# Optimization experiments

Hardware: AMD Instinct MI355X
Metric: run time of the kernel (lower is better)

The kernel has to match this reference:

```python
import jax, jax.numpy as jnp
import numpy as np

EPS_RMS = 1e-6
EPS_L2 = 1e-12  # torch F.normalize default eps


def _l2_normalize(x):
    n = jnp.sqrt(jnp.sum(x * x, axis=-1, keepdims=True))
    return x / jnp.maximum(n, EPS_L2)


def _dwconv(x, w, b):
    # depthwise Conv1d: x [B,L,D], w [D,1,K], b [D]; padding=K//2 (same length for odd K)
    K = w.shape[-1]
    y = jax.lax.conv_general_dilated(
        jnp.swapaxes(x, 1, 2), w, window_strides=(1,),
        padding=[(K // 2, K // 2)], feature_group_count=w.shape[0],
        dimension_numbers=('NCH', 'OIH', 'NCH'))
    return jnp.swapaxes(y + b[None, :, None], 1, 2)


def setup_inputs() -> dict:
    key = jax.random.key(0)
    ks = jax.random.split(key, 12)
    B, L, D, K = 8, 2048, 128, 3
    inp = {
        'x': jax.random.normal(ks[0], (B, L, D), dtype=jnp.float32),
        'state': jnp.zeros((B, D, D), dtype=jnp.float32),
        'W_in': jax.random.normal(ks[1], (4 * D, D), dtype=jnp.float32) * 0.02,
        'W_gate': jax.random.normal(ks[2], (2 * D, D), dtype=jnp.float32) * 0.02,
        'W_out': jax.random.normal(ks[3], (D, D), dtype=jnp.float32) * 0.02,
        'W_res': jax.random.normal(ks[4], (D, D), dtype=jnp.float32) * 0.02,
        'qconv_w': jax.random.normal(ks[5], (D, 1, K), dtype=jnp.float32) * 0.5,
        'qconv_b': jnp.zeros((D,), dtype=jnp.float32),
        'kconv_w': jax.random.normal(ks[6], (D, 1, K), dtype=jnp.float32) * 0.5,
        'kconv_b': jnp.zeros((D,), dtype=jnp.float32),
        'rms_w': jnp.ones((D,), dtype=jnp.float32),
    }
    return inp


def reference(x, state, W_in, W_gate, W_out, W_res,
              qconv_w, qconv_b, kconv_w, kconv_b, rms_w):
    B, L, D = x.shape
    residual = x @ W_res.T
    qkv = x @ W_in.T  # [B,L,4D]
    q, k, v, gate = jnp.split(qkv, 4, axis=-1)
    q = _l2_normalize(jax.nn.sigmoid(_dwconv(q, qconv_w, qconv_b)))
    k = _l2_normalize(jax.nn.sigmoid(_dwconv(k, kconv_w, kconv_b)))
    g = jax.nn.sigmoid(gate @ W_gate.T)  # [B,L,2D]
    alpha, beta = jnp.split(g, 2, axis=-1)

    # Delta-rule recurrence over time. State S [B,D,D] indexed S[b, v_dim, k_dim]:
    # S <- alpha_j * (S_ij - (S k)_i * beta_j k_j) + beta_j * v_i k_j ; out = silu(q @ S)
    def step(S, inp):
        q_t, k_t, v_t, a_t, b_t = inp  # each [B,D]
        Sk = jnp.einsum('bij,bj->bi', S, k_t)          # S @ k
        bk = b_t * k_t                                  # beta*k, column scaling
        S = a_t[:, None, :] * (S - Sk[:, :, None] * bk[:, None, :]) \
            + v_t[:, :, None] * bk[:, None, :]
        out_t = jax.nn.silu(jnp.einsum('bi,bij->bj', q_t, S))
        return S, out_t

    xs = tuple(jnp.swapaxes(a, 0, 1) for a in (q, k, v, alpha, beta))  # [L,B,D]
    S_fin, outs = jax.lax.scan(step, state, xs)
    out = jnp.swapaxes(outs, 0, 1) @ W_out.T  # [B,L,D]
    # dropout (p=0.125) is identity in eval mode
    out = out * jax.lax.rsqrt(jnp.mean(out * out, axis=-1, keepdims=True) + EPS_RMS) * rms_w
    out = out + residual
    return out, S_fin
```

## Files before the change

### kernel.cpp

```cpp
#include <hip/hip_runtime.h>
#include <hip/hip_bf16.h>
#include <math.h>

#define BB 8
#define LL 2048
#define LQ 512
#define DD 128

template <int CTRL>
__device__ __forceinline__ float dpp_add(float x) {
    int xi = __float_as_int(x);
    int yi = __builtin_amdgcn_update_dpp(xi, xi, CTRL, 0xF, 0xF, false);
    return x + __int_as_float(yi);
}
__device__ __forceinline__ float allreduce16(float p) {
    p = dpp_add<0xB1>(p);
    p = dpp_add<0x4E>(p);
    p = dpp_add<0x141>(p);
    p = dpp_add<0x140>(p);
    return p;
}
__device__ __forceinline__ float rlane(float p, int l) {
    return __int_as_float(__builtin_amdgcn_readlane(__float_as_int(p), l));
}

__global__ __launch_bounds__(256) void gemm_kernel(
    const float* __restrict__ X, long ldx, long sB, long sQ,
    const float* __restrict__ W,
    float* __restrict__ C, int ldc,
    int applySig)
{
    __shared__ float Xs[32 * 132];
    __shared__ float Ws[64 * 132];
    const int tid = threadIdx.x;
    const int m0 = blockIdx.x * 32;
    const int o0 = blockIdx.y * 64;
    {
        int row = tid >> 3, cg = tid & 7;
        int m = m0 + row;
        int b = m >> 11, t = m & 2047, qq = t >> 9, tl = t & 511;
        const float* src = X + (size_t)b * sB + (size_t)qq * sQ
                             + (size_t)tl * ldx + cg * 16;
        float* dst = Xs + row * 132 + cg * 16;
#pragma unroll
        for (int u = 0; u < 4; ++u)
            *(float4*)(dst + 4 * u) = *(const float4*)(src + 4 * u);
    }
    {
        int o = tid >> 2, cg = tid & 3;
        const float* src = W + (size_t)(o0 + o) * 128 + cg * 32;
        float* dst = Ws + o * 132 + cg * 32;
#pragma unroll
        for (int u = 0; u < 8; ++u)
            *(float4*)(dst + 4 * u) = *(const float4*)(src + 4 * u);
    }
    __syncthreads();
    const int tx = tid & 31, ty = tid >> 5;
    float acc[4][2] = {};
    const float* xb = Xs + (ty * 4) * 132;
    const float* wb = Ws + (tx * 2) * 132;
    for (int k0 = 0; k0 < 128; k0 += 4) {
        float4 xr[4], wr[2];
#pragma unroll
        for (int r = 0; r < 4; ++r) xr[r] = *(const float4*)(xb + r * 132 + k0);
#pragma unroll
        for (int cc = 0; cc < 2; ++cc) wr[cc] = *(const float4*)(wb + cc * 132 + k0);
#pragma unroll
        for (int r = 0; r < 4; ++r)
#pragma unroll
            for (int cc = 0; cc < 2; ++cc) {
                acc[r][cc] += xr[r].x * wr[cc].x + xr[r].y * wr[cc].y
                            + xr[r].z * wr[cc].z + xr[r].w * wr[cc].w;
            }
    }
#pragma unroll
    for (int r = 0; r < 4; ++r)
#pragma unroll
        for (int cc = 0; cc < 2; ++cc) {
            float v = acc[r][cc];
            if (applySig) v = 1.0f / (1.0f + __expf(-v));
            C[(size_t)(m0 + ty * 4 + r) * ldc + o0 + tx * 2 + cc] = v;
        }
}

__global__ __launch_bounds__(256) void convnorm_kernel(
    const float* __restrict__ qkv,
    const float* __restrict__ qw, const float* __restrict__ qb,
    const float* __restrict__ kw, const float* __restrict__ kb,
    const float* __restrict__ ab,
    float* __restrict__ pack)
{
    const int tid = threadIdx.x;
    const int lane = tid & 63;
    const int wid = tid >> 6;
    const int m = blockIdx.x * 4 + wid;
    const int l = m & (LL - 1);
    const int b = m >> 11;
    const int d0 = lane * 2;
    float yq0 = qb[d0], yq1 = qb[d0 + 1];
    float yk0 = kb[d0], yk1 = kb[d0 + 1];
#pragma unroll
    for (int tau = 0; tau < 3; ++tau) {
        int lp = l + tau - 1;
        if (lp >= 0 && lp < LL) {
            const float* base = qkv + (size_t)(m + tau - 1) * 512;
            yq0 += base[d0]       * qw[d0 * 3 + tau];
            yq1 += base[d0 + 1]   * qw[(d0 + 1) * 3 + tau];
            yk0 += base[128 + d0]     * kw[d0 * 3 + tau];
            yk1 += base[128 + d0 + 1] * kw[(d0 + 1) * 3 + tau];
        }
    }
    yq0 = 1.0f / (1.0f + __expf(-yq0));
    yq1 = 1.0f / (1.0f + __expf(-yq1));
    yk0 = 1.0f / (1.0f + __expf(-yk0));
    yk1 = 1.0f / (1.0f + __expf(-yk1));
    float sq = yq0 * yq0 + yq1 * yq1;
    float sk = yk0 * yk0 + yk1 * yk1;
#pragma unroll
    for (int msk = 1; msk <= 32; msk <<= 1) {
        sq += __shfl_xor(sq, msk);
        sk += __shfl_xor(sk, msk);
    }
    float rq = 1.0f / fmaxf(sqrtf(sq), 1e-12f);
    float rk = 1.0f / fmaxf(sqrtf(sk), 1e-12f);
    float k0n = yk0 * rk, k1n = yk1 * rk;
    float a0 = ab[(size_t)m * 256 + d0];
    float a1 = ab[(size_t)m * 256 + d0 + 1];
    float b0 = ab[(size_t)m * 256 + 128 + d0];
    float b1 = ab[(size_t)m * 256 + 128 + d0 + 1];
    float v0 = qkv[(size_t)m * 512 + 256 + d0];
    float v1 = qkv[(size_t)m * 512 + 256 + d0 + 1];
    float* P = pack + ((size_t)b * 512 + (l >> 2)) * 2560 + (l & 3);
    P[d0 * 4]              = k0n;      P[(d0 + 1) * 4]        = k1n;
    P[512 + d0 * 4]        = b0 * k0n; P[512 + (d0 + 1) * 4]  = b1 * k1n;
    P[1024 + d0 * 4]       = a0;       P[1024 + (d0 + 1) * 4] = a1;
    P[1536 + d0 * 4]       = yq0 * rq; P[1536 + (d0 + 1) * 4] = yq1 * rq;
    P[2048 + d0 * 4]       = v0;       P[2048 + (d0 + 1) * 4] = v1;
}

__global__ __launch_bounds__(64, 1) void recur1_kernel(
    const float* __restrict__ pack, const float* __restrict__ sin,
    __hip_bfloat16* __restrict__ pout, float* __restrict__ sout, int blk0)
{
    const int lane = threadIdx.x;
    const int b = blockIdx.x >> 7;
    const int g = blockIdx.x & 127;
    const int j0 = lane * 2;

    float SA[2];
    {
        const float* sp = sin + ((size_t)b * DD + g) * DD + j0;
        float2 t2 = *(const float2*)sp;
        SA[0] = t2.x; SA[1] = t2.y;
    }

    const float* P = pack + ((size_t)b * 512 + blk0) * 2560;
    __hip_bfloat16* po = pout + ((size_t)g * (BB * LQ) + (size_t)b * LQ) * DD + j0;

    float4 ka4[2][2], ma4[2][2], aa4[2][2];
    float4 qv4[2], vv4[2];

#define PREB(BF)                                                             \
    do {                                                                     \
        ka4[BF][0] = *(const float4*)(P + j0 * 4);                           \
        ka4[BF][1] = *(const float4*)(P + j0 * 4 + 4);                       \
        ma4[BF][0] = *(const float4*)(P + 512 + j0 * 4);                     \
        ma4[BF][1] = *(const float4*)(P + 512 + j0 * 4 + 4);                 \
        aa4[BF][0] = *(const float4*)(P + 1024 + j0 * 4);                    \
        aa4[BF][1] = *(const float4*)(P + 1024 + j0 * 4 + 4);                \
        qv4[BF]    = *(const float4*)(P + 1536 + g * 4);                     \
        vv4[BF]    = *(const float4*)(P + 2048 + g * 4);                     \
        P += 2560;                                                           \
        __builtin_amdgcn_sched_barrier(0);         \
    } while (0)

#define STEPQ(BF, CMP)                                                       \
    do {                                                                     \
        float e = SA[0] * ka4[BF][0].CMP;                                    \
        e = fmaf(SA[1], ka4[BF][1].CMP, e);                                  \
        float p = allreduce16(e);                                            \
        float sk = (rlane(p, 0) + rlane(p, 16))                              \
                 + (rlane(p, 32) + rlane(p, 48));                            \
        float vg = vv4[BF].CMP, qg = qv4[BF].CMP;                            \
        float a0 = aa4[BF][0].CMP, a1 = aa4[BF][1].CMP;                      \
        float w0 = fmaf(-a0, sk, vg);                                        \
        SA[0] = fmaf(ma4[BF][0].CMP, w0, a0 * SA[0]);                        \
        float w1 = fmaf(-a1, sk, vg);                                        \
        SA[1] = fmaf(ma4[BF][1].CMP, w1, a1 * SA[1]);                        \
        __hip_bfloat162 h2;                                                  \
        h2.x = __float2bfloat16(qg * SA[0]);                                 \
        h2.y = __float2bfloat16(qg * SA[1]);                                 \
        *(__hip_bfloat162*)po = h2;                                          \
        po += DD;                                                            \
    } while (0)

#define STEP4(BF) \
    do { STEPQ(BF, x); STEPQ(BF, y); STEPQ(BF, z); STEPQ(BF, w); } while (0)

    PREB(0);
    PREB(1);
    for (int tb = 0; tb < LQ / 4; tb += 2) {
        STEP4(0);
        PREB(0);
        STEP4(1);
        PREB(1);
    }
#undef PREB
#undef STEPQ
#undef STEP4

    {
        float* sp = sout + ((size_t)b * DD + g) * DD + j0;
        float2 o2 = {SA[0], SA[1]};
        *(float2*)sp = o2;
    }
}

__global__ __launch_bounds__(256) void combine_silu_kernel(
    const ushort* __restrict__ pout, float* __restrict__ ocbase, int q)
{
    const size_t NQ = (size_t)BB * LQ * DD;
    size_t idx = ((size_t)blockIdx.x * 256 + threadIdx.x) * 4;
    float s0 = 0, s1 = 0, s2 = 0, s3 = 0;
#pragma unroll 8
    for (int gi = 0; gi < 128; ++gi) {
        uint2 u = *(const uint2*)(pout + gi * NQ + idx);
        s0 += __uint_as_float((u.x & 0xffffu) << 16);
        s1 += __uint_as_float(u.x & 0xffff0000u);
        s2 += __uint_as_float((u.y & 0xffffu) << 16);
        s3 += __uint_as_float(u.y & 0xffff0000u);
    }
    float4 r;
    r.x = s0 / (1.0f + __expf(-s0));
    r.y = s1 / (1.0f + __expf(-s1));
    r.z = s2 / (1.0f + __expf(-s2));
    r.w = s3 / (1.0f + __expf(-s3));
    size_t b = idx >> 16;
    size_t rem = idx & ((size_t)LQ * DD - 1);
    float* dst = ocbase + b * (512ull * 2560) + (size_t)q * (128ull * 2560) + rem;
    *(float4*)dst = r;
}

__global__ __launch_bounds__(256) void rms_res_kernel(
    const float* __restrict__ y, const float* __restrict__ res,
    const float* __restrict__ rmsw, float* __restrict__ out)
{
    const int tid = threadIdx.x;
    const int lane = tid & 63;
    const int wid = tid >> 6;
    const int m = blockIdx.x * 4 + wid;
    const int d0 = lane * 2;
    size_t o = (size_t)m * DD + d0;
    float2 yv = *(const float2*)(y + o);
    float ss = yv.x * yv.x + yv.y * yv.y;
#pragma unroll
    for (int msk = 1; msk <= 32; msk <<= 1) ss += __shfl_xor(ss, msk);
    float r = rsqrtf(ss * (1.0f / 128.0f) + 1e-6f);
    float2 rv = *(const float2*)(res + o);
    out[o]     = yv.x * r * rmsw[d0]     + rv.x;
    out[o + 1] = yv.y * r * rmsw[d0 + 1] + rv.y;
}

extern "C" void kernel_launch(void* const* d_in, const int* in_sizes, int n_in,
                              void* d_out, int out_size, void* d_ws, size_t ws_size,
                              hipStream_t stream)
{
    const float* x      = (const float*)d_in[0];
    const float* state  = (const float*)d_in[1];
    const float* W_in   = (const float*)d_in[2];
    const float* W_gate = (const float*)d_in[3];
    const float* W_out  = (const float*)d_in[4];
    const float* W_res  = (const float*)d_in[5];
    const float* qcw    = (const float*)d_in[6];
    const float* qcb    = (const float*)d_in[7];
    const float* kcw    = (const float*)d_in[8];
    const float* kcb    = (const float*)d_in[9];
    const float* rmsw   = (const float*)d_in[10];
    float* out  = (float*)d_out;
    float* sfin = out + (size_t)BB * LL * DD;

    const size_t M = (size_t)BB * LL;
    char* base = (char*)d_ws;
    const size_t PACK_BYTES = M * 640 * 4;
    float* pack = (float*)base;
    char*  poreg = base + PACK_BYTES;
    float* qkv = (float*)poreg;
    float* abv = (float*)(poreg + M * 512 * 4);
    __hip_bfloat16* po = (__hip_bfloat16*)poreg;
    float* res = (float*)poreg;
    float* yb  = (float*)(poreg + M * DD * 4);

    dim3 blk(256);
    gemm_kernel<<<dim3(M / 32, 8), blk, 0, stream>>>(
        x, 128, 2048L * 128, 512L * 128, W_in, qkv, 512, 0);
    gemm_kernel<<<dim3(M / 32, 4), blk, 0, stream>>>(
        qkv + 384, 512, 2048L * 512, 512L * 512, W_gate, abv, 256, 1);
    convnorm_kernel<<<dim3(M / 4), blk, 0, stream>>>(qkv, qcw, qcb, kcw, kcb, abv, pack);
    for (int q = 0; q < 4; ++q) {
        const float* sin = (q == 0) ? state : sfin;
        recur1_kernel<<<dim3(BB * 128), dim3(64), 0, stream>>>(
            pack, sin, po, sfin, q * 128);
        combine_silu_kernel<<<dim3(512), blk, 0, stream>>>(
            (const ushort*)po, pack, q);
    }
    gemm_kernel<<<dim3(M / 32, 2), blk, 0, stream>>>(
        x, 128, 2048L * 128, 512L * 128, W_res, res, 128, 0);
    gemm_kernel<<<dim3(M / 32, 2), blk, 0, stream>>>(
        pack, 128, 512L * 2560, 128L * 2560, W_out, yb, 128, 0);
    rms_res_kernel<<<dim3(M / 4), blk, 0, stream>>>(yb, res, rmsw, out);
}
```

Baseline: 562.7 us.

## Process two state rows per wave and split recurrence into two halves

The recurrence kernel now has each 64-lane block own two rows of the state instead of one, so 512 blocks run in place of 1024. Each k/alpha/beta load and each step's bookkeeping is shared across both rows, and the two rows' partial outputs are summed before the bf16 store. The sequence is cut into 2 chunks of 1024 steps instead of 4 chunks of 512, which halves the recurrence and combine launches and halves the partial-output buffer the combine kernel reads. In exchange there is less block-level parallelism and a longer serial dependence chain per launch. Chunk and stride indexing in the GEMM and combine kernels are updated to match.

```diff
diff --git a/kernel.cpp b/kernel.cpp
--- a/kernel.cpp
+++ b/kernel.cpp
@@ -4,7 +4,7 @@
 
 #define BB 8
 #define LL 2048
-#define LQ 512
+#define LH 1024
 #define DD 128
 
 template <int CTRL>
@@ -25,7 +25,7 @@
 }
 
 __global__ __launch_bounds__(256) void gemm_kernel(
-    const float* __restrict__ X, long ldx, long sB, long sQ,
+    const float* __restrict__ X, long ldx, long sB, long sH,
     const float* __restrict__ W,
     float* __restrict__ C, int ldc,
     int applySig)
@@ -38,8 +38,8 @@
     {
         int row = tid >> 3, cg = tid & 7;
         int m = m0 + row;
-        int b = m >> 11, t = m & 2047, qq = t >> 9, tl = t & 511;
-        const float* src = X + (size_t)b * sB + (size_t)qq * sQ
+        int b = m >> 11, t = m & 2047, h = t >> 10, tl = t & 1023;
+        const float* src = X + (size_t)b * sB + (size_t)h * sH
                              + (size_t)tl * ldx + cg * 16;
         float* dst = Xs + row * 132 + cg * 16;
 #pragma unroll
@@ -138,27 +138,31 @@
     P[2048 + d0 * 4]       = v0;       P[2048 + (d0 + 1) * 4] = v1;
 }
 
-__global__ __launch_bounds__(64, 1) void recur1_kernel(
+__global__ __launch_bounds__(64, 1) void recur2c_kernel(
     const float* __restrict__ pack, const float* __restrict__ sin,
     __hip_bfloat16* __restrict__ pout, float* __restrict__ sout, int blk0)
 {
     const int lane = threadIdx.x;
-    const int b = blockIdx.x >> 7;
-    const int g = blockIdx.x & 127;
+    const int b = blockIdx.x >> 6;
+    const int g = blockIdx.x & 63;
+    const int r0 = g * 2;
     const int j0 = lane * 2;
 
-    float SA[2];
+    float S0[2], S1[2];
     {
-        const float* sp = sin + ((size_t)b * DD + g) * DD + j0;
+        const float* sp = sin + ((size_t)b * DD + r0) * DD + j0;
         float2 t2 = *(const float2*)sp;
-        SA[0] = t2.x; SA[1] = t2.y;
+        S0[0] = t2.x; S0[1] = t2.y;
+        sp += DD;
+        t2 = *(const float2*)sp;
+        S1[0] = t2.x; S1[1] = t2.y;
     }
 
     const float* P = pack + ((size_t)b * 512 + blk0) * 2560;
-    __hip_bfloat16* po = pout + ((size_t)g * (BB * LQ) + (size_t)b * LQ) * DD + j0;
+    __hip_bfloat16* po = pout + ((size_t)g * (BB * LH) + (size_t)b * LH) * DD + j0;
 
     float4 ka4[2][2], ma4[2][2], aa4[2][2];
-    float4 qv4[2], vv4[2];
+    float4 qv4[2][2], vv4[2][2];
 
 #define PREB(BF)                                                             \
     do {                                                                     \
@@ -168,28 +172,38 @@
         ma4[BF][1] = *(const float4*)(P + 512 + j0 * 4 + 4);                 \
         aa4[BF][0] = *(const float4*)(P + 1024 + j0 * 4);                    \
         aa4[BF][1] = *(const float4*)(P + 1024 + j0 * 4 + 4);                \
-        qv4[BF]    = *(const float4*)(P + 1536 + g * 4);                     \
-        vv4[BF]    = *(const float4*)(P + 2048 + g * 4);                     \
+        qv4[BF][0] = *(const float4*)(P + 1536 + r0 * 4);                    \
+        qv4[BF][1] = *(const float4*)(P + 1536 + r0 * 4 + 4);                \
+        vv4[BF][0] = *(const float4*)(P + 2048 + r0 * 4);                    \
+        vv4[BF][1] = *(const float4*)(P + 2048 + r0 * 4 + 4);                \
         P += 2560;                                                           \
         __builtin_amdgcn_sched_barrier(0);         \
     } while (0)
 
 #define STEPQ(BF, CMP)                                                       \
     do {                                                                     \
-        float e = SA[0] * ka4[BF][0].CMP;                                    \
-        e = fmaf(SA[1], ka4[BF][1].CMP, e);                                  \
-        float p = allreduce16(e);                                            \
-        float sk = (rlane(p, 0) + rlane(p, 16))                              \
-                 + (rlane(p, 32) + rlane(p, 48));                            \
-        float vg = vv4[BF].CMP, qg = qv4[BF].CMP;                            \
+        float k0 = ka4[BF][0].CMP, k1 = ka4[BF][1].CMP;                      \
+        float e0 = S0[0] * k0; e0 = fmaf(S0[1], k1, e0);                     \
+        float e1 = S1[0] * k0; e1 = fmaf(S1[1], k1, e1);                     \
+        float p0 = allreduce16(e0);                                          \
+        float p1 = allreduce16(e1);                                          \
+        float sk0 = (rlane(p0, 0) + rlane(p0, 16))                           \
+                  + (rlane(p0, 32) + rlane(p0, 48));                         \
+        float sk1 = (rlane(p1, 0) + rlane(p1, 16))                           \
+                  + (rlane(p1, 32) + rlane(p1, 48));                         \
+        float v0 = vv4[BF][0].CMP, v1 = vv4[BF][1].CMP;                      \
+        float q0 = qv4[BF][0].CMP, q1 = qv4[BF][1].CMP;                      \
         float a0 = aa4[BF][0].CMP, a1 = aa4[BF][1].CMP;                      \
-        float w0 = fmaf(-a0, sk, vg);                                        \
-        SA[0] = fmaf(ma4[BF][0].CMP, w0, a0 * SA[0]);                        \
-        float w1 = fmaf(-a1, sk, vg);                                        \
-        SA[1] = fmaf(ma4[BF][1].CMP, w1, a1 * SA[1]);                        \
+        float m0 = ma4[BF][0].CMP, m1 = ma4[BF][1].CMP;                      \
+        float t00 = fmaf(-a0, sk0, v0); S0[0] = fmaf(m0, t00, a0 * S0[0]);   \
+        float t10 = fmaf(-a0, sk1, v1); S1[0] = fmaf(m0, t10, a0 * S1[0]);   \
+        float t01 = fmaf(-a1, sk0, v0); S0[1] = fmaf(m1, t01, a1 * S0[1]);   \
+        float t11 = fmaf(-a1, sk1, v1); S1[1] = fmaf(m1, t11, a1 * S1[1]);   \
+        float po0 = fmaf(q1, S1[0], q0 * S0[0]);                             \
+        float po1 = fmaf(q1, S1[1], q0 * S0[1]);                             \
         __hip_bfloat162 h2;                                                  \
-        h2.x = __float2bfloat16(qg * SA[0]);                                 \
-        h2.y = __float2bfloat16(qg * SA[1]);                                 \
+        h2.x = __float2bfloat16(po0);                                        \
+        h2.y = __float2bfloat16(po1);                                        \
         *(__hip_bfloat162*)po = h2;                                          \
         po += DD;                                                            \
     } while (0)
@@ -199,7 +213,7 @@
 
     PREB(0);
     PREB(1);
-    for (int tb = 0; tb < LQ / 4; tb += 2) {
+    for (int tb = 0; tb < LH / 4; tb += 2) {
         STEP4(0);
         PREB(0);
         STEP4(1);
@@ -210,21 +224,24 @@
 #undef STEP4
 
     {
-        float* sp = sout + ((size_t)b * DD + g) * DD + j0;
-        float2 o2 = {SA[0], SA[1]};
+        float* sp = sout + ((size_t)b * DD + r0) * DD + j0;
+        float2 o2 = {S0[0], S0[1]};
         *(float2*)sp = o2;
+        sp += DD;
+        float2 o3 = {S1[0], S1[1]};
+        *(float2*)sp = o3;
     }
 }
 
 __global__ __launch_bounds__(256) void combine_silu_kernel(
-    const ushort* __restrict__ pout, float* __restrict__ ocbase, int q)
-{
-    const size_t NQ = (size_t)BB * LQ * DD;
+    const ushort* __restrict__ pout, float* __restrict__ ocbase, int h)
+{
+    const size_t NHALF = (size_t)BB * LH * DD;
     size_t idx = ((size_t)blockIdx.x * 256 + threadIdx.x) * 4;
     float s0 = 0, s1 = 0, s2 = 0, s3 = 0;
 #pragma unroll 8
-    for (int gi = 0; gi < 128; ++gi) {
-        uint2 u = *(const uint2*)(pout + gi * NQ + idx);
+    for (int gi = 0; gi < 64; ++gi) {
+        uint2 u = *(const uint2*)(pout + gi * NHALF + idx);
         s0 += __uint_as_float((u.x & 0xffffu) << 16);
         s1 += __uint_as_float(u.x & 0xffff0000u);
         s2 += __uint_as_float((u.y & 0xffffu) << 16);
@@ -235,9 +252,9 @@
     r.y = s1 / (1.0f + __expf(-s1));
     r.z = s2 / (1.0f + __expf(-s2));
     r.w = s3 / (1.0f + __expf(-s3));
-    size_t b = idx >> 16;
-    size_t rem = idx & ((size_t)LQ * DD - 1);
-    float* dst = ocbase + b * (512ull * 2560) + (size_t)q * (128ull * 2560) + rem;
+    size_t b = idx >> 17;
+    size_t rem = idx & ((size_t)LH * DD - 1);
+    float* dst = ocbase + b * (2048ull * 640) + (size_t)h * (1024ull * 640) + rem;
     *(float4*)dst = r;
 }
 
@@ -290,22 +307,22 @@
     float* res = (float*)poreg;
     float* yb  = (float*)(poreg + M * DD * 4);
 
+    const long ld128 = 128, ld512 = 512;
     dim3 blk(256);
     gemm_kernel<<<dim3(M / 32, 8), blk, 0, stream>>>(
-        x, 128, 2048L * 128, 512L * 128, W_in, qkv, 512, 0);
+        x, ld128, 2048 * ld128, 1024 * ld128, W_in, qkv, 512, 0);
     gemm_kernel<<<dim3(M / 32, 4), blk, 0, stream>>>(
-        qkv + 384, 512, 2048L * 512, 512L * 512, W_gate, abv, 256, 1);
+        qkv + 384, ld512, 2048 * ld512, 1024 * ld512, W_gate, abv, 256, 1);
     convnorm_kernel<<<dim3(M / 4), blk, 0, stream>>>(qkv, qcw, qcb, kcw, kcb, abv, pack);
-    for (int q = 0; q < 4; ++q) {
-        const float* sin = (q == 0) ? state : sfin;
-        recur1_kernel<<<dim3(BB * 128), dim3(64), 0, stream>>>(
-            pack, sin, po, sfin, q * 128);
-        combine_silu_kernel<<<dim3(512), blk, 0, stream>>>(
-            (const ushort*)po, pack, q);
-    }
+    recur2c_kernel<<<dim3(BB * 64), dim3(64), 0, stream>>>(pack, state, po, sfin, 0);
+    combine_silu_kernel<<<dim3((BB * LH * DD) / 1024), blk, 0, stream>>>(
+        (const ushort*)po, pack, 0);
+    recur2c_kernel<<<dim3(BB * 64), dim3(64), 0, stream>>>(pack, sfin, po, sfin, 256);
+    combine_silu_kernel<<<dim3((BB * LH * DD) / 1024), blk, 0, stream>>>(
+        (const ushort*)po, pack, 1);
     gemm_kernel<<<dim3(M / 32, 2), blk, 0, stream>>>(
-        x, 128, 2048L * 128, 512L * 128, W_res, res, 128, 0);
+        x, ld128, 2048 * ld128, 1024 * ld128, W_res, res, 128, 0);
     gemm_kernel<<<dim3(M / 32, 2), blk, 0, stream>>>(
-        pack, 128, 512L * 2560, 128L * 2560, W_out, yb, 128, 0);
+        pack, ld128, 2048 * 640, 1024 * 640, W_out, yb, 128, 0);
     rms_res_kernel<<<dim3(M / 4), blk, 0, stream>>>(yb, res, rmsw, out);
 }
```

New measurement: 612.3 us. 8.8% more time.

## Stream recurrence inputs into LDS with async global_load_lds triple buffering

Applied to the files above, without the earlier changes.

The recurrence kernel no longer double-buffers per-step inputs in registers. It now issues asynchronous global-to-LDS DMA loads into a three-slot LDS ring, waits on vmcnt by hand, and reads each block back from LDS right before computing. The aim is to free vector registers and keep the loads two blocks ahead of the serial dependency chain. The min-blocks launch bound is also dropped, which may change register allocation and occupancy. In exchange, each iteration adds LDS read latency, relies on hand-coded waitcnt values that also count the output stores, and prefetches two blocks past the end of each quarter.

```diff
diff --git a/kernel.cpp b/kernel.cpp
--- a/kernel.cpp
+++ b/kernel.cpp
@@ -22,6 +22,11 @@
 }
 __device__ __forceinline__ float rlane(float p, int l) {
     return __int_as_float(__builtin_amdgcn_readlane(__float_as_int(p), l));
+}
+__device__ __forceinline__ void dma16(const float* g, char* l) {
+    __builtin_amdgcn_global_load_lds(
+        (const __attribute__((address_space(1))) void*)g,
+        (__attribute__((address_space(3))) void*)l, 16, 0, 0);
 }
 
 __global__ __launch_bounds__(256) void gemm_kernel(
@@ -138,10 +143,11 @@
     P[2048 + d0 * 4]       = v0;       P[2048 + (d0 + 1) * 4] = v1;
 }
 
-__global__ __launch_bounds__(64, 1) void recur1_kernel(
+__global__ __launch_bounds__(64) void recur1_kernel(
     const float* __restrict__ pack, const float* __restrict__ sin,
     __hip_bfloat16* __restrict__ pout, float* __restrict__ sout, int blk0)
 {
+    __shared__ __attribute__((aligned(16))) char smem[3 * 8192];
     const int lane = threadIdx.x;
     const int b = blockIdx.x >> 7;
     const int g = blockIdx.x & 127;
@@ -154,39 +160,36 @@
         SA[0] = t2.x; SA[1] = t2.y;
     }
 
-    const float* P = pack + ((size_t)b * 512 + blk0) * 2560;
+    const float* P0 = pack + ((size_t)b * 512 + blk0) * 2560;
     __hip_bfloat16* po = pout + ((size_t)g * (BB * LQ) + (size_t)b * LQ) * DD + j0;
 
-    float4 ka4[2][2], ma4[2][2], aa4[2][2];
-    float4 qv4[2], vv4[2];
-
-#define PREB(BF)                                                             \
+#define DMABLK(BUF, OFF)                                                     \
     do {                                                                     \
-        ka4[BF][0] = *(const float4*)(P + j0 * 4);                           \
-        ka4[BF][1] = *(const float4*)(P + j0 * 4 + 4);                       \
-        ma4[BF][0] = *(const float4*)(P + 512 + j0 * 4);                     \
-        ma4[BF][1] = *(const float4*)(P + 512 + j0 * 4 + 4);                 \
-        aa4[BF][0] = *(const float4*)(P + 1024 + j0 * 4);                    \
-        aa4[BF][1] = *(const float4*)(P + 1024 + j0 * 4 + 4);                \
-        qv4[BF]    = *(const float4*)(P + 1536 + g * 4);                     \
-        vv4[BF]    = *(const float4*)(P + 2048 + g * 4);                     \
-        P += 2560;                                                           \
-        __builtin_amdgcn_sched_barrier(0);         \
+        char* L = smem + (BUF) * 8192;                                       \
+        const float* G = P0 + (size_t)(OFF) * 2560;                          \
+        dma16(G + lane * 8,              L + 0);                             \
+        dma16(G + lane * 8 + 4,          L + 1024);                          \
+        dma16(G + 512 + lane * 8,        L + 2048);                          \
+        dma16(G + 512 + lane * 8 + 4,    L + 3072);                          \
+        dma16(G + 1024 + lane * 8,       L + 4096);                          \
+        dma16(G + 1024 + lane * 8 + 4,   L + 5120);                          \
+        dma16(G + 1536 + g * 4,          L + 6144);                          \
+        dma16(G + 2048 + g * 4,          L + 7168);                          \
     } while (0)
 
-#define STEPQ(BF, CMP)                                                       \
+#define STEPQ(CMP)                                                           \
     do {                                                                     \
-        float e = SA[0] * ka4[BF][0].CMP;                                    \
-        e = fmaf(SA[1], ka4[BF][1].CMP, e);                                  \
+        float e = SA[0] * k_lo.CMP;                                          \
+        e = fmaf(SA[1], k_hi.CMP, e);                                        \
         float p = allreduce16(e);                                            \
         float sk = (rlane(p, 0) + rlane(p, 16))                              \
                  + (rlane(p, 32) + rlane(p, 48));                            \
-        float vg = vv4[BF].CMP, qg = qv4[BF].CMP;                            \
-        float a0 = aa4[BF][0].CMP, a1 = aa4[BF][1].CMP;                      \
+        float vg = v4.CMP, qg = q4.CMP;                                      \
+        float a0 = a_lo.CMP, a1 = a_hi.CMP;                                  \
         float w0 = fmaf(-a0, sk, vg);                                        \
-        SA[0] = fmaf(ma4[BF][0].CMP, w0, a0 * SA[0]);                        \
+        SA[0] = fmaf(m_lo.CMP, w0, a0 * SA[0]);                              \
         float w1 = fmaf(-a1, sk, vg);                                        \
-        SA[1] = fmaf(ma4[BF][1].CMP, w1, a1 * SA[1]);                        \
+        SA[1] = fmaf(m_hi.CMP, w1, a1 * SA[1]);                              \
         __hip_bfloat162 h2;                                                  \
         h2.x = __float2bfloat16(qg * SA[0]);                                 \
         h2.y = __float2bfloat16(qg * SA[1]);                                 \
@@ -194,20 +197,30 @@
         po += DD;                                                            \
     } while (0)
 
-#define STEP4(BF) \
-    do { STEPQ(BF, x); STEPQ(BF, y); STEPQ(BF, z); STEPQ(BF, w); } while (0)
-
-    PREB(0);
-    PREB(1);
-    for (int tb = 0; tb < LQ / 4; tb += 2) {
-        STEP4(0);
-        PREB(0);
-        STEP4(1);
-        PREB(1);
-    }
-#undef PREB
+    DMABLK(0, 0);
+    DMABLK(1, 1);
+
+    for (int tb = 0; tb < LQ / 4; ++tb) {
+        if (tb == 0) __builtin_amdgcn_s_waitcnt(0x0F78);
+        else         __builtin_amdgcn_s_waitcnt(0x0F7C);
+        __builtin_amdgcn_sched_barrier(0);
+        const char* Lc = smem + (tb % 3) * 8192;
+        float4 k_lo = *(const float4*)(Lc + lane * 16);
+        float4 k_hi = *(const float4*)(Lc + 1024 + lane * 16);
+        float4 m_lo = *(const float4*)(Lc + 2048 + lane * 16);
+        float4 m_hi = *(const float4*)(Lc + 3072 + lane * 16);
+        float4 a_lo = *(const float4*)(Lc + 4096 + lane * 16);
+        float4 a_hi = *(const float4*)(Lc + 5120 + lane * 16);
+        float4 q4   = *(const float4*)(Lc + 6144 + lane * 16);
+        float4 v4   = *(const float4*)(Lc + 7168 + lane * 16);
+        __builtin_amdgcn_sched_barrier(0);
+        DMABLK((tb + 2) % 3, tb + 2);
+        __builtin_amdgcn_sched_barrier(0);
+        STEPQ(x); STEPQ(y); STEPQ(z); STEPQ(w);
+        __builtin_amdgcn_sched_barrier(0);
+    }
+#undef DMABLK
 #undef STEPQ
-#undef STEP4
 
     {
         float* sp = sout + ((size_t)b * DD + g) * DD + j0;
```

New measurement: 679.1 us. 1.21x slower.
